# Performance work log

Hardware: AMD Instinct MI355X
Metric: run time of the kernel (lower is better)

The kernel has to match this reference:

```python
import jax, jax.numpy as jnp
import numpy as np

N_NODES = 100000
N_EDGES = 1600000
D_IN = 128
D_OUT = 128


def setup_inputs() -> dict:
    key = jax.random.key(0)
    k1, k2, k3, k4 = jax.random.split(key, 4)
    feat = jax.random.normal(k1, (N_NODES, D_IN), dtype=jnp.float32)
    weight = jax.random.normal(k2, (D_IN, D_OUT), dtype=jnp.float32) * (1.0 / np.sqrt(D_IN))
    src = jax.random.randint(k3, (N_EDGES,), 0, N_NODES, dtype=jnp.int64)
    dst = jax.random.randint(k4, (N_EDGES,), 0, N_NODES, dtype=jnp.int64)
    return {"feat": feat, "weight": weight, "src": src, "dst": dst}


def reference(feat, weight, src, dst):
    n = feat.shape[0]
    ones = jnp.ones(src.shape[0], dtype=feat.dtype)
    # norm == 'both': scale source features by out_degree^{-1/2}
    out_deg = jnp.clip(jax.ops.segment_sum(ones, src, num_segments=n), 1.0)
    feat_src = feat * (out_deg ** -0.5)[:, None]  # [N, D_in]
    # update_all(copy_src, sum): gather src features, segment-sum into dst
    agg = jax.ops.segment_sum(feat_src[src], dst, num_segments=n)  # [N, D_in]
    # dense transform with external weight
    rst = agg @ weight  # [N, D_out]
    # destination-side normalization by in_degree^{-1/2}
    in_deg = jnp.clip(jax.ops.segment_sum(ones, dst, num_segments=n), 1.0)
    rst = rst * (in_deg ** -0.5)[:, None]
    return rst
```

## Files before the change

kernel.cpp:

```cpp
#include <hip/hip_runtime.h>
#include <stdint.h>


#define DIM 128
#define PN 128
#define MAXPP 800
#define CAPE 2560
#define CAPS 2560
#define PT 512
#define EPT 13
#define CHUNK (PT * EPT)
#define CAPA 1536

typedef unsigned int uint;
typedef unsigned short ushortT;

__device__ __forceinline__ ushortT f2bf(float x) {
    uint u = __float_as_uint(x);
    u = (u + 0x7FFFu + ((u >> 16) & 1u)) >> 16;
    return (ushortT)u;
}
__device__ __forceinline__ float bf2f(ushortT b) {
    return __uint_as_float(((uint)b) << 16);
}

__global__ __launch_bounds__(PT) void part(
    const int* __restrict__ src, const int* __restrict__ dst,
    int* __restrict__ curD, int* __restrict__ curS,
    int* __restrict__ pairs, unsigned char* __restrict__ srcb,
    int E, int NPP) {
    __shared__ int cD[MAXPP], cS[MAXPP];
    __shared__ int lofD[MAXPP], lofS[MAXPP];
    __shared__ int gbD[MAXPP], gbS[MAXPP];
    __shared__ int bufD[CHUNK];
    __shared__ unsigned char bufS[CHUNK];

    int tid = threadIdx.x;
    long long base = (long long)blockIdx.x * CHUNK;
    for (int i = tid; i < NPP; i += PT) { cD[i] = 0; cS[i] = 0; }
    __syncthreads();

    int sv[EPT], dv[EPT], lrD[EPT], lrS[EPT];
#pragma unroll
    for (int j = 0; j < EPT; ++j) {
        long long e = base + tid + j * PT;
        bool ok = e < E;
        int s = 0, d = 0;
        if (ok) { s = src[e]; d = dst[e]; }
        sv[j] = s; dv[j] = d;
        lrD[j] = ok ? atomicAdd(&cD[d >> 7], 1) : 0;
        lrS[j] = ok ? atomicAdd(&cS[s >> 7], 1) : 0;
    }
    __syncthreads();

    int* sc = bufD;
    for (int pass = 0; pass < 2; ++pass) {
        const int* cnts = pass ? cS : cD;
        int* lof = pass ? lofS : lofD;
        for (int i = tid; i < 1024; i += PT) sc[i] = (i < NPP) ? cnts[i] : 0;
        __syncthreads();
        for (int off = 1; off < 1024; off <<= 1) {
            int i0 = tid, i1 = tid + PT;
            int a0 = (i0 >= off) ? sc[i0 - off] : 0;
            int a1 = (i1 >= off) ? sc[i1 - off] : 0;
            __syncthreads();
            sc[i0] += a0; sc[i1] += a1;
            __syncthreads();
        }
        for (int i = tid; i < NPP; i += PT) lof[i] = sc[i] - cnts[i];
        __syncthreads();
    }

    for (int i = tid; i < NPP; i += PT) {
        int c = cD[i];
        gbD[i] = c ? atomicAdd(&curD[i], c) : 0;
        c = cS[i];
        gbS[i] = c ? atomicAdd(&curS[i], c) : 0;
    }

#pragma unroll
    for (int j = 0; j < EPT; ++j) {
        long long e = base + tid + j * PT;
        if (e < E) {
            int s = sv[j], d = dv[j];
            bufD[lofD[d >> 7] + lrD[j]] = (s << 7) | (d & 127);
            bufS[lofS[s >> 7] + lrS[j]] = (unsigned char)(s & 127);
        }
    }
    __syncthreads();

    int cnt = (int)(((long long)E - base < (long long)CHUNK) ? (E - base) : CHUNK);
    for (int i = tid; i < cnt; i += PT) {
        int lo = 0, hi = NPP - 1;
        while (lo < hi) { int mid = (lo + hi + 1) >> 1; if (lofD[mid] <= i) lo = mid; else hi = mid - 1; }
        int pos = gbD[lo] + (i - lofD[lo]);
        if (pos < CAPE) pairs[(size_t)lo * CAPE + pos] = bufD[i];
    }
    for (int i = tid; i < cnt; i += PT) {
        int lo = 0, hi = NPP - 1;
        while (lo < hi) { int mid = (lo + hi + 1) >> 1; if (lofS[mid] <= i) lo = mid; else hi = mid - 1; }
        int pos = gbS[lo] + (i - lofS[lo]);
        if (pos < CAPS) srcb[(size_t)lo * CAPS + pos] = bufS[i];
    }
}

__global__ __launch_bounds__(256) void deg(
    const int* __restrict__ curS, const unsigned char* __restrict__ srcb,
    float* __restrict__ oscale, int N) {
    __shared__ int hist[PN];
    int p = blockIdx.x, tid = threadIdx.x;
    if (tid < PN) hist[tid] = 0;
    __syncthreads();
    int cnt = min(curS[p], CAPS);
    const unsigned char* b = &srcb[(size_t)p * CAPS];
    for (int i = tid; i < cnt; i += 256) atomicAdd(&hist[b[i]], 1);
    __syncthreads();
    if (tid < PN) {
        int node = p * PN + tid;
        if (node < N) oscale[node] = rsqrtf((float)max(hist[tid], 1));
    }
}

__global__ __launch_bounds__(256) void gemm_h(
    const float* __restrict__ feat, const float* __restrict__ W,
    const float* __restrict__ oscale, ushortT* __restrict__ h, int M) {
    __shared__ float As[32][36];
    __shared__ float Bs[32][128];

    int tid = threadIdx.x;
    int m0 = blockIdx.x * 32;
    int tx = tid & 31;
    int ty = tid >> 5;
    int bc = tx << 2;

    float acc[4][4];
#pragma unroll
    for (int r = 0; r < 4; ++r)
#pragma unroll
        for (int c = 0; c < 4; ++c) acc[r][c] = 0.f;

    int am = tid >> 3;
    int ak = (tid & 7) << 2;
    int arow = m0 + am;
    float scale = (arow < M) ? oscale[arow] : 0.f;

    for (int k0 = 0; k0 < DIM; k0 += 32) {
        float4 a = make_float4(0.f, 0.f, 0.f, 0.f);
        if (arow < M) a = *(const float4*)&feat[(size_t)arow * DIM + k0 + ak];
        As[ak + 0][am] = a.x * scale;
        As[ak + 1][am] = a.y * scale;
        As[ak + 2][am] = a.z * scale;
        As[ak + 3][am] = a.w * scale;
#pragma unroll
        for (int i = 0; i < 4; ++i) {
            int k = ty + i * 8;
            *(float4*)&Bs[k][bc] = *(const float4*)&W[(size_t)(k0 + k) * DIM + bc];
        }
        __syncthreads();
#pragma unroll
        for (int k = 0; k < 32; ++k) {
            float4 a4 = *(const float4*)&As[k][ty << 2];
            float4 b4 = *(const float4*)&Bs[k][bc];
            acc[0][0] += a4.x * b4.x; acc[0][1] += a4.x * b4.y; acc[0][2] += a4.x * b4.z; acc[0][3] += a4.x * b4.w;
            acc[1][0] += a4.y * b4.x; acc[1][1] += a4.y * b4.y; acc[1][2] += a4.y * b4.z; acc[1][3] += a4.y * b4.w;
            acc[2][0] += a4.z * b4.x; acc[2][1] += a4.z * b4.y; acc[2][2] += a4.z * b4.z; acc[2][3] += a4.z * b4.w;
            acc[3][0] += a4.w * b4.x; acc[3][1] += a4.w * b4.y; acc[3][2] += a4.w * b4.z; acc[3][3] += a4.w * b4.w;
        }
        __syncthreads();
    }
    float* T = &Bs[0][0];
#pragma unroll
    for (int r = 0; r < 4; ++r)
#pragma unroll
        for (int j = 0; j < 4; ++j)
            T[((ty << 2) + r) * 128 + bc + j] = acc[r][j];
    __syncthreads();
    for (int q = tid; q < 1024; q += 256) {
        int row = q >> 5, l = q & 31;
        int m = m0 + row;
        if (m < M) {
            ushort4 v;
            v.x = f2bf(T[row * 128 + l]);
            v.y = f2bf(T[row * 128 + l + 32]);
            v.z = f2bf(T[row * 128 + l + 64]);
            v.w = f2bf(T[row * 128 + l + 96]);
            *(ushort4*)&h[(size_t)m * DIM + (l << 2)] = v;
        }
    }
}

__global__ __launch_bounds__(256) void aggp(
    const ushortT* __restrict__ h, const int* __restrict__ pairs,
    const int* __restrict__ curD, float* __restrict__ out, int N) {
    __shared__ int sorted[CAPA];
    __shared__ int hist[64], offs[64], cur[64];
    int b = blockIdx.x;
    int p = b >> 1, sub = b & 1;
    int tid = threadIdx.x;
    if (tid < 64) hist[tid] = 0;
    __syncthreads();
    int cnt = min(curD[p], CAPE);
    const int* pb = &pairs[(size_t)p * CAPE];
    for (int i = tid; i < cnt; i += 256) {
        int dl = pb[i] & 127;
        if ((dl >> 6) == sub) atomicAdd(&hist[dl & 63], 1);
    }
    __syncthreads();
    if (tid < 64) {
        int x = hist[tid], incl = x;
        for (int o = 1; o < 64; o <<= 1) {
            int y = __shfl_up(incl, o, 64);
            if (tid >= o) incl += y;
        }
        offs[tid] = incl - x;
        cur[tid] = incl - x;
    }
    __syncthreads();
    for (int i = tid; i < cnt; i += 256) {
        int w = pb[i];
        int dl = w & 127;
        if ((dl >> 6) == sub) {
            int slot = atomicAdd(&cur[dl & 63], 1);
            if (slot < CAPA) sorted[slot] = w >> 7;
        }
    }
    __syncthreads();
    int hw = tid >> 5, l = tid & 31;
    for (int nd = hw; nd < 64; nd += 8) {
        int node = p * PN + sub * 64 + nd;
        if (node >= N) continue;
        int start = offs[nd];
        int degn = hist[nd];
        int end = min(start + degn, CAPA);
        float a0 = 0.f, a1 = 0.f, a2 = 0.f, a3 = 0.f;
        int e = start;
        for (; e + 8 <= end; e += 8) {
            int s0 = sorted[e],     s1 = sorted[e + 1];
            int s2 = sorted[e + 2], s3 = sorted[e + 3];
            int s4 = sorted[e + 4], s5 = sorted[e + 5];
            int s6 = sorted[e + 6], s7 = sorted[e + 7];
            ushort4 v0 = *(const ushort4*)&h[(size_t)s0 * DIM + (l << 2)];
            ushort4 v1 = *(const ushort4*)&h[(size_t)s1 * DIM + (l << 2)];
            ushort4 v2 = *(const ushort4*)&h[(size_t)s2 * DIM + (l << 2)];
            ushort4 v3 = *(const ushort4*)&h[(size_t)s3 * DIM + (l << 2)];
            ushort4 v4 = *(const ushort4*)&h[(size_t)s4 * DIM + (l << 2)];
            ushort4 v5 = *(const ushort4*)&h[(size_t)s5 * DIM + (l << 2)];
            ushort4 v6 = *(const ushort4*)&h[(size_t)s6 * DIM + (l << 2)];
            ushort4 v7 = *(const ushort4*)&h[(size_t)s7 * DIM + (l << 2)];
            a0 += ((bf2f(v0.x) + bf2f(v1.x)) + (bf2f(v2.x) + bf2f(v3.x))) +
                  ((bf2f(v4.x) + bf2f(v5.x)) + (bf2f(v6.x) + bf2f(v7.x)));
            a1 += ((bf2f(v0.y) + bf2f(v1.y)) + (bf2f(v2.y) + bf2f(v3.y))) +
                  ((bf2f(v4.y) + bf2f(v5.y)) + (bf2f(v6.y) + bf2f(v7.y)));
            a2 += ((bf2f(v0.z) + bf2f(v1.z)) + (bf2f(v2.z) + bf2f(v3.z))) +
                  ((bf2f(v4.z) + bf2f(v5.z)) + (bf2f(v6.z) + bf2f(v7.z)));
            a3 += ((bf2f(v0.w) + bf2f(v1.w)) + (bf2f(v2.w) + bf2f(v3.w))) +
                  ((bf2f(v4.w) + bf2f(v5.w)) + (bf2f(v6.w) + bf2f(v7.w)));
        }
        for (; e < end; ++e) {
            int s0 = sorted[e];
            ushort4 v0 = *(const ushort4*)&h[(size_t)s0 * DIM + (l << 2)];
            a0 += bf2f(v0.x); a1 += bf2f(v0.y);
            a2 += bf2f(v0.z); a3 += bf2f(v0.w);
        }
        float scn = rsqrtf((float)max(degn, 1));
        size_t ob = (size_t)node * DIM;
        out[ob + l]      = a0 * scn;
        out[ob + l + 32] = a1 * scn;
        out[ob + l + 64] = a2 * scn;
        out[ob + l + 96] = a3 * scn;
    }
}

extern "C" void kernel_launch(void* const* d_in, const int* in_sizes, int n_in,
                              void* d_out, int out_size, void* d_ws, size_t ws_size,
                              hipStream_t stream) {
    const float* feat = (const float*)d_in[0];
    const float* W    = (const float*)d_in[1];
    const int*   src  = (const int*)d_in[2];
    const int*   dst  = (const int*)d_in[3];
    float* out = (float*)d_out;

    int N = in_sizes[0] / DIM;
    int E = in_sizes[2];
    int NPP = (N + PN - 1) / PN;

    int* curD = (int*)d_ws;
    int* curS = curD + NPP;
    float* oscale = (float*)(curS + NPP);
    int* pairs = (int*)(oscale + N);
    unsigned char* srcb = (unsigned char*)(pairs + (size_t)NPP * CAPE);
    uintptr_t hp = (uintptr_t)(srcb + (size_t)NPP * CAPS);
    ushortT* h = (ushortT*)((hp + 15) & ~(uintptr_t)15);

    hipMemsetAsync(curD, 0, (size_t)2 * NPP * sizeof(int), stream);

    int nb = (E + CHUNK - 1) / CHUNK;
    part<<<nb, PT, 0, stream>>>(src, dst, curD, curS, pairs, srcb, E, NPP);
    deg<<<NPP, 256, 0, stream>>>(curS, srcb, oscale, N);
    gemm_h<<<(N + 31) / 32, 256, 0, stream>>>(feat, W, oscale, h, N);
    aggp<<<2 * NPP, 256, 0, stream>>>(h, pairs, curD, out, N);
}
```

Before: 278.6 us.

## Use split-bf16 MFMA GEMM, global atomic out-degree, and wider aggregation loads

The scalar fp32 GEMM becomes an MFMA bf16 GEMM. Inputs and weights are split into hi/lo bf16 parts and combined with three MFMAs to keep near-fp32 accuracy, and a new small kernel pre-transposes the weights into a swizzled layout. Out-degree is now counted with global atomics during partitioning, which removes the source bucketing pass and the separate degree kernel. The aggregation kernel switches to 16-lane groups with 16-byte loads per neighbour row. The global atomics on random source nodes add contention in exchange for less partition work.

```diff
diff --git a/kernel.cpp b/kernel.cpp
--- a/kernel.cpp
+++ b/kernel.cpp
@@ -6,7 +6,6 @@
 #define PN 128
 #define MAXPP 800
 #define CAPE 2560
-#define CAPS 2560
 #define PT 512
 #define EPT 13
 #define CHUNK (PT * EPT)
@@ -14,6 +13,8 @@
 
 typedef unsigned int uint;
 typedef unsigned short ushortT;
+typedef __attribute__((ext_vector_type(8))) short bf16x8;
+typedef __attribute__((ext_vector_type(4))) float f32x4;
 
 __device__ __forceinline__ ushortT f2bf(float x) {
     uint u = __float_as_uint(x);
@@ -23,168 +24,190 @@
 __device__ __forceinline__ float bf2f(ushortT b) {
     return __uint_as_float(((uint)b) << 16);
 }
+__device__ __forceinline__ float bflo(uint u) { return __uint_as_float(u << 16); }
+__device__ __forceinline__ float bfhi(uint u) { return __uint_as_float(u & 0xffff0000u); }
 
 __global__ __launch_bounds__(PT) void part(
     const int* __restrict__ src, const int* __restrict__ dst,
-    int* __restrict__ curD, int* __restrict__ curS,
-    int* __restrict__ pairs, unsigned char* __restrict__ srcb,
-    int E, int NPP) {
-    __shared__ int cD[MAXPP], cS[MAXPP];
-    __shared__ int lofD[MAXPP], lofS[MAXPP];
-    __shared__ int gbD[MAXPP], gbS[MAXPP];
+    int* __restrict__ curD, int* __restrict__ cnt,
+    int* __restrict__ pairs, int E, int NPP) {
+    __shared__ int cD[MAXPP], lofD[MAXPP], gbD[MAXPP];
     __shared__ int bufD[CHUNK];
-    __shared__ unsigned char bufS[CHUNK];
 
     int tid = threadIdx.x;
     long long base = (long long)blockIdx.x * CHUNK;
-    for (int i = tid; i < NPP; i += PT) { cD[i] = 0; cS[i] = 0; }
-    __syncthreads();
-
-    int sv[EPT], dv[EPT], lrD[EPT], lrS[EPT];
+    for (int i = tid; i < NPP; i += PT) cD[i] = 0;
+    __syncthreads();
+
+    int sv[EPT], dv[EPT], lrD[EPT];
 #pragma unroll
     for (int j = 0; j < EPT; ++j) {
         long long e = base + tid + j * PT;
         bool ok = e < E;
         int s = 0, d = 0;
-        if (ok) { s = src[e]; d = dst[e]; }
+        if (ok) { s = src[e]; d = dst[e]; atomicAdd(&cnt[s], 1); }
         sv[j] = s; dv[j] = d;
         lrD[j] = ok ? atomicAdd(&cD[d >> 7], 1) : 0;
-        lrS[j] = ok ? atomicAdd(&cS[s >> 7], 1) : 0;
     }
     __syncthreads();
 
     int* sc = bufD;
-    for (int pass = 0; pass < 2; ++pass) {
-        const int* cnts = pass ? cS : cD;
-        int* lof = pass ? lofS : lofD;
-        for (int i = tid; i < 1024; i += PT) sc[i] = (i < NPP) ? cnts[i] : 0;
+    for (int i = tid; i < 1024; i += PT) sc[i] = (i < NPP) ? cD[i] : 0;
+    __syncthreads();
+    for (int off = 1; off < 1024; off <<= 1) {
+        int i0 = tid, i1 = tid + PT;
+        int a0 = (i0 >= off) ? sc[i0 - off] : 0;
+        int a1 = (i1 >= off) ? sc[i1 - off] : 0;
         __syncthreads();
-        for (int off = 1; off < 1024; off <<= 1) {
-            int i0 = tid, i1 = tid + PT;
-            int a0 = (i0 >= off) ? sc[i0 - off] : 0;
-            int a1 = (i1 >= off) ? sc[i1 - off] : 0;
-            __syncthreads();
-            sc[i0] += a0; sc[i1] += a1;
-            __syncthreads();
-        }
-        for (int i = tid; i < NPP; i += PT) lof[i] = sc[i] - cnts[i];
+        sc[i0] += a0; sc[i1] += a1;
         __syncthreads();
     }
+    for (int i = tid; i < NPP; i += PT) lofD[i] = sc[i] - cD[i];
+    __syncthreads();
 
     for (int i = tid; i < NPP; i += PT) {
         int c = cD[i];
         gbD[i] = c ? atomicAdd(&curD[i], c) : 0;
-        c = cS[i];
-        gbS[i] = c ? atomicAdd(&curS[i], c) : 0;
     }
 
 #pragma unroll
     for (int j = 0; j < EPT; ++j) {
         long long e = base + tid + j * PT;
-        if (e < E) {
-            int s = sv[j], d = dv[j];
-            bufD[lofD[d >> 7] + lrD[j]] = (s << 7) | (d & 127);
-            bufS[lofS[s >> 7] + lrS[j]] = (unsigned char)(s & 127);
-        }
-    }
-    __syncthreads();
-
-    int cnt = (int)(((long long)E - base < (long long)CHUNK) ? (E - base) : CHUNK);
-    for (int i = tid; i < cnt; i += PT) {
+        if (e < E) bufD[lofD[dv[j] >> 7] + lrD[j]] = (sv[j] << 7) | (dv[j] & 127);
+    }
+    __syncthreads();
+
+    int cntE = (int)(((long long)E - base < (long long)CHUNK) ? (E - base) : CHUNK);
+    for (int i = tid; i < cntE; i += PT) {
         int lo = 0, hi = NPP - 1;
         while (lo < hi) { int mid = (lo + hi + 1) >> 1; if (lofD[mid] <= i) lo = mid; else hi = mid - 1; }
         int pos = gbD[lo] + (i - lofD[lo]);
         if (pos < CAPE) pairs[(size_t)lo * CAPE + pos] = bufD[i];
     }
-    for (int i = tid; i < cnt; i += PT) {
-        int lo = 0, hi = NPP - 1;
-        while (lo < hi) { int mid = (lo + hi + 1) >> 1; if (lofS[mid] <= i) lo = mid; else hi = mid - 1; }
-        int pos = gbS[lo] + (i - lofS[lo]);
-        if (pos < CAPS) srcb[(size_t)lo * CAPS + pos] = bufS[i];
-    }
-}
-
-__global__ __launch_bounds__(256) void deg(
-    const int* __restrict__ curS, const unsigned char* __restrict__ srcb,
-    float* __restrict__ oscale, int N) {
-    __shared__ int hist[PN];
-    int p = blockIdx.x, tid = threadIdx.x;
-    if (tid < PN) hist[tid] = 0;
-    __syncthreads();
-    int cnt = min(curS[p], CAPS);
-    const unsigned char* b = &srcb[(size_t)p * CAPS];
-    for (int i = tid; i < cnt; i += 256) atomicAdd(&hist[b[i]], 1);
-    __syncthreads();
-    if (tid < PN) {
-        int node = p * PN + tid;
-        if (node < N) oscale[node] = rsqrtf((float)max(hist[tid], 1));
-    }
+}
+
+__global__ __launch_bounds__(256) void wtr(const float* __restrict__ W,
+                                           ushortT* __restrict__ Bt) {
+    __shared__ float Ws[32][132];
+    int tid = threadIdx.x;
+    int k0 = blockIdx.x * 32;
+    for (int i = tid; i < 1024; i += 256) {
+        int r = i >> 5, cc = (i & 31) << 2;
+        *(float4*)&Ws[r][cc] = *(const float4*)&W[(size_t)(k0 + r) * DIM + cc];
+    }
+    __syncthreads();
+    int n = tid >> 1, ks = (tid & 1) << 4;
+    ushortT th[16], tl[16];
+#pragma unroll
+    for (int j = 0; j < 16; ++j) {
+        float w = Ws[ks + j][n];
+        th[j] = f2bf(w);
+        tl[j] = f2bf(w - bf2f(th[j]));
+    }
+    uint oh[8], ol[8];
+#pragma unroll
+    for (int j = 0; j < 8; ++j) {
+        oh[j] = (uint)th[2 * j] | ((uint)th[2 * j + 1] << 16);
+        ol[j] = (uint)tl[2 * j] | ((uint)tl[2 * j + 1] << 16);
+    }
+    ushortT* bh = &Bt[(size_t)n * DIM + k0 + ks];
+    ushortT* bl = bh + DIM * DIM;
+    *(uint4*)bh = *(uint4*)&oh[0];
+    *(uint4*)(bh + 8) = *(uint4*)&oh[4];
+    *(uint4*)bl = *(uint4*)&ol[0];
+    *(uint4*)(bl + 8) = *(uint4*)&ol[4];
 }
 
 __global__ __launch_bounds__(256) void gemm_h(
-    const float* __restrict__ feat, const float* __restrict__ W,
-    const float* __restrict__ oscale, ushortT* __restrict__ h, int M) {
-    __shared__ float As[32][36];
-    __shared__ float Bs[32][128];
+    const float* __restrict__ feat, const ushortT* __restrict__ Bt,
+    const int* __restrict__ cnt, ushortT* __restrict__ h, int M) {
+    __shared__ __align__(16) ushortT Bs[2][128 * 128];
 
     int tid = threadIdx.x;
-    int m0 = blockIdx.x * 32;
-    int tx = tid & 31;
-    int ty = tid >> 5;
-    int bc = tx << 2;
-
-    float acc[4][4];
-#pragma unroll
-    for (int r = 0; r < 4; ++r)
-#pragma unroll
-        for (int c = 0; c < 4; ++c) acc[r][c] = 0.f;
-
-    int am = tid >> 3;
-    int ak = (tid & 7) << 2;
-    int arow = m0 + am;
-    float scale = (arow < M) ? oscale[arow] : 0.f;
-
-    for (int k0 = 0; k0 < DIM; k0 += 32) {
-        float4 a = make_float4(0.f, 0.f, 0.f, 0.f);
-        if (arow < M) a = *(const float4*)&feat[(size_t)arow * DIM + k0 + ak];
-        As[ak + 0][am] = a.x * scale;
-        As[ak + 1][am] = a.y * scale;
-        As[ak + 2][am] = a.z * scale;
-        As[ak + 3][am] = a.w * scale;
-#pragma unroll
-        for (int i = 0; i < 4; ++i) {
-            int k = ty + i * 8;
-            *(float4*)&Bs[k][bc] = *(const float4*)&W[(size_t)(k0 + k) * DIM + bc];
-        }
-        __syncthreads();
-#pragma unroll
-        for (int k = 0; k < 32; ++k) {
-            float4 a4 = *(const float4*)&As[k][ty << 2];
-            float4 b4 = *(const float4*)&Bs[k][bc];
-            acc[0][0] += a4.x * b4.x; acc[0][1] += a4.x * b4.y; acc[0][2] += a4.x * b4.z; acc[0][3] += a4.x * b4.w;
-            acc[1][0] += a4.y * b4.x; acc[1][1] += a4.y * b4.y; acc[1][2] += a4.y * b4.z; acc[1][3] += a4.y * b4.w;
-            acc[2][0] += a4.z * b4.x; acc[2][1] += a4.z * b4.y; acc[2][2] += a4.z * b4.z; acc[2][3] += a4.z * b4.w;
-            acc[3][0] += a4.w * b4.x; acc[3][1] += a4.w * b4.y; acc[3][2] += a4.w * b4.z; acc[3][3] += a4.w * b4.w;
-        }
-        __syncthreads();
-    }
-    float* T = &Bs[0][0];
-#pragma unroll
-    for (int r = 0; r < 4; ++r)
-#pragma unroll
-        for (int j = 0; j < 4; ++j)
-            T[((ty << 2) + r) * 128 + bc + j] = acc[r][j];
-    __syncthreads();
-    for (int q = tid; q < 1024; q += 256) {
-        int row = q >> 5, l = q & 31;
-        int m = m0 + row;
-        if (m < M) {
-            ushort4 v;
-            v.x = f2bf(T[row * 128 + l]);
-            v.y = f2bf(T[row * 128 + l + 32]);
-            v.z = f2bf(T[row * 128 + l + 64]);
-            v.w = f2bf(T[row * 128 + l + 96]);
-            *(ushort4*)&h[(size_t)m * DIM + (l << 2)] = v;
+    for (int i = tid; i < 4096; i += 256) {
+        int pl = i >> 11, r = (i >> 4) & 127, s = i & 15;
+        uint4 v = *(const uint4*)&Bt[(size_t)i << 3];
+        *(uint4*)&Bs[pl][r * 128 + ((s << 3) ^ ((r & 7) << 3))] = v;
+    }
+
+    int wid = tid >> 6;
+    int l = tid & 63;
+    int lr = l & 15;
+    int lk = l >> 4;
+    int m0 = blockIdx.x * 128;
+    int row0 = m0 + wid * 32 + lr;
+    int row1 = row0 + 16;
+    bool ok0 = row0 < M, ok1 = row1 < M;
+    float sc0 = ok0 ? rsqrtf((float)max(cnt[row0], 1)) : 0.f;
+    float sc1 = ok1 ? rsqrtf((float)max(cnt[row1], 1)) : 0.f;
+    const float* fp0 = feat + (size_t)(ok0 ? row0 : 0) * DIM;
+    const float* fp1 = feat + (size_t)(ok1 ? row1 : 0) * DIM;
+
+    f32x4 acc[2][8];
+    f32x4 z = {0.f, 0.f, 0.f, 0.f};
+#pragma unroll
+    for (int m = 0; m < 2; ++m)
+#pragma unroll
+        for (int n = 0; n < 8; ++n) acc[m][n] = z;
+
+    __syncthreads();
+
+#pragma unroll
+    for (int kc = 0; kc < 4; ++kc) {
+        int kb = kc * 32 + lk * 8;
+        float4 x0 = *(const float4*)&fp0[kb];
+        float4 x1 = *(const float4*)&fp0[kb + 4];
+        float4 y0 = *(const float4*)&fp1[kb];
+        float4 y1 = *(const float4*)&fp1[kb + 4];
+        bf16x8 ah0, al0, ah1, al1;
+        {
+            float f[8] = {x0.x * sc0, x0.y * sc0, x0.z * sc0, x0.w * sc0,
+                          x1.x * sc0, x1.y * sc0, x1.z * sc0, x1.w * sc0};
+#pragma unroll
+            for (int j = 0; j < 8; ++j) {
+                ushortT hh = f2bf(f[j]);
+                ah0[j] = (short)hh;
+                al0[j] = (short)f2bf(f[j] - bf2f(hh));
+            }
+        }
+        {
+            float f[8] = {y0.x * sc1, y0.y * sc1, y0.z * sc1, y0.w * sc1,
+                          y1.x * sc1, y1.y * sc1, y1.z * sc1, y1.w * sc1};
+#pragma unroll
+            for (int j = 0; j < 8; ++j) {
+                ushortT hh = f2bf(f[j]);
+                ah1[j] = (short)hh;
+                al1[j] = (short)f2bf(f[j] - bf2f(hh));
+            }
+        }
+#pragma unroll
+        for (int n = 0; n < 8; ++n) {
+            int brow = n * 16 + lr;
+            int bidx = brow * 128 + (kb ^ ((brow & 7) << 3));
+            bf16x8 bh = *(const bf16x8*)&Bs[0][bidx];
+            bf16x8 bl = *(const bf16x8*)&Bs[1][bidx];
+            acc[0][n] = __builtin_amdgcn_mfma_f32_16x16x32_bf16(ah0, bh, acc[0][n], 0, 0, 0);
+            acc[1][n] = __builtin_amdgcn_mfma_f32_16x16x32_bf16(ah1, bh, acc[1][n], 0, 0, 0);
+            acc[0][n] = __builtin_amdgcn_mfma_f32_16x16x32_bf16(al0, bh, acc[0][n], 0, 0, 0);
+            acc[1][n] = __builtin_amdgcn_mfma_f32_16x16x32_bf16(al1, bh, acc[1][n], 0, 0, 0);
+            acc[0][n] = __builtin_amdgcn_mfma_f32_16x16x32_bf16(ah0, bl, acc[0][n], 0, 0, 0);
+            acc[1][n] = __builtin_amdgcn_mfma_f32_16x16x32_bf16(ah1, bl, acc[1][n], 0, 0, 0);
+        }
+    }
+
+#pragma unroll
+    for (int m = 0; m < 2; ++m) {
+#pragma unroll
+        for (int r = 0; r < 4; ++r) {
+            int row = m0 + wid * 32 + m * 16 + lk * 4 + r;
+            if (row < M) {
+                uint w0 = (uint)f2bf(acc[m][0][r]) | ((uint)f2bf(acc[m][1][r]) << 16);
+                uint w1 = (uint)f2bf(acc[m][2][r]) | ((uint)f2bf(acc[m][3][r]) << 16);
+                uint w2 = (uint)f2bf(acc[m][4][r]) | ((uint)f2bf(acc[m][5][r]) << 16);
+                uint w3 = (uint)f2bf(acc[m][6][r]) | ((uint)f2bf(acc[m][7][r]) << 16);
+                uint4 o = make_uint4(w0, w1, w2, w3);
+                *(uint4*)&h[(size_t)row * DIM + (lr << 3)] = o;
+            }
         }
     }
 }
@@ -225,49 +248,64 @@
         }
     }
     __syncthreads();
-    int hw = tid >> 5, l = tid & 31;
-    for (int nd = hw; nd < 64; nd += 8) {
+    int g = tid >> 4, c = tid & 15;
+    int cb = c << 3;
+    for (int nd = g; nd < 64; nd += 16) {
         int node = p * PN + sub * 64 + nd;
         if (node >= N) continue;
         int start = offs[nd];
         int degn = hist[nd];
         int end = min(start + degn, CAPA);
         float a0 = 0.f, a1 = 0.f, a2 = 0.f, a3 = 0.f;
+        float a4 = 0.f, a5 = 0.f, a6 = 0.f, a7 = 0.f;
         int e = start;
         for (; e + 8 <= end; e += 8) {
             int s0 = sorted[e],     s1 = sorted[e + 1];
             int s2 = sorted[e + 2], s3 = sorted[e + 3];
             int s4 = sorted[e + 4], s5 = sorted[e + 5];
             int s6 = sorted[e + 6], s7 = sorted[e + 7];
-            ushort4 v0 = *(const ushort4*)&h[(size_t)s0 * DIM + (l << 2)];
-            ushort4 v1 = *(const ushort4*)&h[(size_t)s1 * DIM + (l << 2)];
-            ushort4 v2 = *(const ushort4*)&h[(size_t)s2 * DIM + (l << 2)];
-            ushort4 v3 = *(const ushort4*)&h[(size_t)s3 * DIM + (l << 2)];
-            ushort4 v4 = *(const ushort4*)&h[(size_t)s4 * DIM + (l << 2)];
-            ushort4 v5 = *(const ushort4*)&h[(size_t)s5 * DIM + (l << 2)];
-            ushort4 v6 = *(const ushort4*)&h[(size_t)s6 * DIM + (l << 2)];
-            ushort4 v7 = *(const ushort4*)&h[(size_t)s7 * DIM + (l << 2)];
-            a0 += ((bf2f(v0.x) + bf2f(v1.x)) + (bf2f(v2.x) + bf2f(v3.x))) +
-                  ((bf2f(v4.x) + bf2f(v5.x)) + (bf2f(v6.x) + bf2f(v7.x)));
-            a1 += ((bf2f(v0.y) + bf2f(v1.y)) + (bf2f(v2.y) + bf2f(v3.y))) +
-                  ((bf2f(v4.y) + bf2f(v5.y)) + (bf2f(v6.y) + bf2f(v7.y)));
-            a2 += ((bf2f(v0.z) + bf2f(v1.z)) + (bf2f(v2.z) + bf2f(v3.z))) +
-                  ((bf2f(v4.z) + bf2f(v5.z)) + (bf2f(v6.z) + bf2f(v7.z)));
-            a3 += ((bf2f(v0.w) + bf2f(v1.w)) + (bf2f(v2.w) + bf2f(v3.w))) +
-                  ((bf2f(v4.w) + bf2f(v5.w)) + (bf2f(v6.w) + bf2f(v7.w)));
+            uint4 v0 = *(const uint4*)&h[(size_t)s0 * DIM + cb];
+            uint4 v1 = *(const uint4*)&h[(size_t)s1 * DIM + cb];
+            uint4 v2 = *(const uint4*)&h[(size_t)s2 * DIM + cb];
+            uint4 v3 = *(const uint4*)&h[(size_t)s3 * DIM + cb];
+            uint4 v4 = *(const uint4*)&h[(size_t)s4 * DIM + cb];
+            uint4 v5 = *(const uint4*)&h[(size_t)s5 * DIM + cb];
+            uint4 v6 = *(const uint4*)&h[(size_t)s6 * DIM + cb];
+            uint4 v7 = *(const uint4*)&h[(size_t)s7 * DIM + cb];
+            a0 += ((bflo(v0.x) + bflo(v1.x)) + (bflo(v2.x) + bflo(v3.x))) +
+                  ((bflo(v4.x) + bflo(v5.x)) + (bflo(v6.x) + bflo(v7.x)));
+            a1 += ((bfhi(v0.x) + bfhi(v1.x)) + (bfhi(v2.x) + bfhi(v3.x))) +
+                  ((bfhi(v4.x) + bfhi(v5.x)) + (bfhi(v6.x) + bfhi(v7.x)));
+            a2 += ((bflo(v0.y) + bflo(v1.y)) + (bflo(v2.y) + bflo(v3.y))) +
+                  ((bflo(v4.y) + bflo(v5.y)) + (bflo(v6.y) + bflo(v7.y)));
+            a3 += ((bfhi(v0.y) + bfhi(v1.y)) + (bfhi(v2.y) + bfhi(v3.y))) +
+                  ((bfhi(v4.y) + bfhi(v5.y)) + (bfhi(v6.y) + bfhi(v7.y)));
+            a4 += ((bflo(v0.z) + bflo(v1.z)) + (bflo(v2.z) + bflo(v3.z))) +
+                  ((bflo(v4.z) + bflo(v5.z)) + (bflo(v6.z) + bflo(v7.z)));
+            a5 += ((bfhi(v0.z) + bfhi(v1.z)) + (bfhi(v2.z) + bfhi(v3.z))) +
+                  ((bfhi(v4.z) + bfhi(v5.z)) + (bfhi(v6.z) + bfhi(v7.z)));
+            a6 += ((bflo(v0.w) + bflo(v1.w)) + (bflo(v2.w) + bflo(v3.w))) +
+                  ((bflo(v4.w) + bflo(v5.w)) + (bflo(v6.w) + bflo(v7.w)));
+            a7 += ((bfhi(v0.w) + bfhi(v1.w)) + (bfhi(v2.w) + bfhi(v3.w))) +
+                  ((bfhi(v4.w) + bfhi(v5.w)) + (bfhi(v6.w) + bfhi(v7.w)));
         }
         for (; e < end; ++e) {
-            int s0 = sorted[e];
-            ushort4 v0 = *(const ushort4*)&h[(size_t)s0 * DIM + (l << 2)];
-            a0 += bf2f(v0.x); a1 += bf2f(v0.y);
-            a2 += bf2f(v0.z); a3 += bf2f(v0.w);
+            uint4 v = *(const uint4*)&h[(size_t)sorted[e] * DIM + cb];
+            a0 += bflo(v.x); a1 += bfhi(v.x);
+            a2 += bflo(v.y); a3 += bfhi(v.y);
+            a4 += bflo(v.z); a5 += bfhi(v.z);
+            a6 += bflo(v.w); a7 += bfhi(v.w);
         }
         float scn = rsqrtf((float)max(degn, 1));
-        size_t ob = (size_t)node * DIM;
-        out[ob + l]      = a0 * scn;
-        out[ob + l + 32] = a1 * scn;
-        out[ob + l + 64] = a2 * scn;
-        out[ob + l + 96] = a3 * scn;
+        size_t ob = (size_t)node * DIM + c;
+        out[ob]       = a0 * scn;
+        out[ob + 16]  = a1 * scn;
+        out[ob + 32]  = a2 * scn;
+        out[ob + 48]  = a3 * scn;
+        out[ob + 64]  = a4 * scn;
+        out[ob + 80]  = a5 * scn;
+        out[ob + 96]  = a6 * scn;
+        out[ob + 112] = a7 * scn;
     }
 }
 
@@ -285,18 +323,17 @@
     int NPP = (N + PN - 1) / PN;
 
     int* curD = (int*)d_ws;
-    int* curS = curD + NPP;
-    float* oscale = (float*)(curS + NPP);
-    int* pairs = (int*)(oscale + N);
-    unsigned char* srcb = (unsigned char*)(pairs + (size_t)NPP * CAPE);
-    uintptr_t hp = (uintptr_t)(srcb + (size_t)NPP * CAPS);
-    ushortT* h = (ushortT*)((hp + 15) & ~(uintptr_t)15);
-
-    hipMemsetAsync(curD, 0, (size_t)2 * NPP * sizeof(int), stream);
-
+    int* cnt  = curD + NPP;
+    int* pairs = cnt + N;
+    uintptr_t bp = (uintptr_t)(pairs + (size_t)NPP * CAPE);
+    ushortT* Bt = (ushortT*)((bp + 15) & ~(uintptr_t)15);
+    ushortT* h = Bt + 2 * DIM * DIM;
+
+    hipMemsetAsync(curD, 0, (size_t)(NPP + N) * sizeof(int), stream);
+
+    wtr<<<4, 256, 0, stream>>>(W, Bt);
     int nb = (E + CHUNK - 1) / CHUNK;
-    part<<<nb, PT, 0, stream>>>(src, dst, curD, curS, pairs, srcb, E, NPP);
-    deg<<<NPP, 256, 0, stream>>>(curS, srcb, oscale, N);
-    gemm_h<<<(N + 31) / 32, 256, 0, stream>>>(feat, W, oscale, h, N);
+    part<<<nb, PT, 0, stream>>>(src, dst, curD, cnt, pairs, E, NPP);
+    gemm_h<<<(N + 127) / 128, 256, 0, stream>>>(feat, Bt, cnt, h, N);
     aggp<<<2 * NPP, 256, 0, stream>>>(h, pairs, curD, out, N);
 }
```

Result: slower. 296.7 us (+6.5%).
